# Performance work log

Measured on AMD Instinct MI355X. Metric: run time of the kernel, lower is better.

The kernel has to match this reference:

```python
import jax, jax.numpy as jnp
import numpy as np

K = 20          # neighbors
EPS = 1e-5      # BatchNorm eps (eval mode, running_mean=0, running_var=1)
SLOPE = 0.01    # LeakyReLU default negative_slope


def lrelu(v):
    return jnp.where(v >= 0, v, SLOPE * v)


def bn4d(y, g, b):  # y: (B, C, N, k) or (B, C, N)
    shape = (1, g.shape[0]) + (1,) * (y.ndim - 2)
    return y * (g / jnp.sqrt(1.0 + EPS)).reshape(shape) + b.reshape(shape)


def knn_idx(x, k):  # x: (B, C, N) -> (B, N, k) indices of k nearest points
    xx = jnp.sum(x * x, axis=1)                      # (B, N)
    inner = jnp.einsum('bcn,bcm->bnm', x, x)         # (B, N, N)
    dist = 2.0 * inner - xx[:, :, None] - xx[:, None, :]  # = -||xi-xj||^2
    _, idx = jax.lax.top_k(dist, k)
    return idx


def graph_feature(x, k):  # x: (B, C, N) -> (B, 2C, N, k)
    idx = knn_idx(x, k)                              # (B, N, k)
    xt = jnp.transpose(x, (0, 2, 1))                 # (B, N, C)
    nbr = jax.vmap(lambda p, i: p[i])(xt, idx)       # (B, N, k, C) gather
    ctr = xt[:, :, None, :]                          # (B, N, 1, C)
    feat = jnp.concatenate([nbr - ctr, jnp.broadcast_to(ctr, nbr.shape)], axis=-1)
    return jnp.transpose(feat, (0, 3, 1, 2))         # (B, 2C, N, k)


def edge_conv(x, w, g, b, bias=None):  # 1x1 conv + BN(eval) + LeakyReLU + max over k
    f = graph_feature(x, K)                          # (B, 2C, N, k)
    y = jnp.einsum('oc,bcnk->bonk', w, f)
    if bias is not None:
        y = y + bias.reshape(1, -1, 1, 1)
    return jnp.max(lrelu(bn4d(y, g, b)), axis=-1)    # (B, O, N)


def setup_inputs() -> dict:
    key = jax.random.key(0)
    ks = jax.random.split(key, 24)
    W = lambda k_, o, c: jax.random.normal(k_, (o, c), jnp.float32) / np.sqrt(c)
    g = lambda k_, c: 1.0 + 0.1 * jax.random.normal(k_, (c,), jnp.float32)
    bt = lambda k_, c: 0.1 * jax.random.normal(k_, (c,), jnp.float32)
    return {
        'x': jax.random.normal(ks[0], (8, 1024, 3), jnp.float32),
        'conv1_w': W(ks[1], 64, 6), 'conv1_b': bt(ks[2], 64),
        'bn1_g': g(ks[3], 64), 'bn1_b': bt(ks[4], 64),
        'conv2_w': W(ks[5], 64, 128), 'bn2_g': g(ks[6], 64), 'bn2_b': bt(ks[7], 64),
        'conv3_w': W(ks[8], 128, 128), 'bn3_g': g(ks[9], 128), 'bn3_b': bt(ks[10], 128),
        'conv4_w': W(ks[11], 256, 256), 'bn4_g': g(ks[12], 256), 'bn4_b': bt(ks[13], 256),
        'conv5_w': W(ks[14], 1024, 512),
        'lin1_w': W(ks[15], 512, 1024), 'bn6_g': g(ks[16], 512), 'bn6_b': bt(ks[17], 512),
        'lin2_w': W(ks[18], 256, 512), 'lin2_b': bt(ks[19], 256),
        'bn7_g': g(ks[20], 256), 'bn7_b': bt(ks[21], 256),
        'lin3_w': W(ks[22], 40, 256), 'lin3_b': bt(ks[23], 40),
    }


def reference(x, conv1_w, conv1_b, bn1_g, bn1_b, conv2_w, bn2_g, bn2_b,
              conv3_w, bn3_g, bn3_b, conv4_w, bn4_g, bn4_b, conv5_w,
              lin1_w, bn6_g, bn6_b, lin2_w, lin2_b, bn7_g, bn7_b, lin3_w, lin3_b):
    p = jnp.transpose(x, (0, 2, 1))                  # (B, 3, N)
    x1 = edge_conv(p, conv1_w, bn1_g, bn1_b, bias=conv1_b)   # (B, 64, N)
    x2 = edge_conv(x1, conv2_w, bn2_g, bn2_b)                # (B, 64, N)
    x3 = edge_conv(x2, conv3_w, bn3_g, bn3_b)                # (B, 128, N)
    x4 = edge_conv(x3, conv4_w, bn4_g, bn4_b)                # (B, 256, N)
    xc = jnp.concatenate([x1, x2, x3, x4], axis=1)           # (B, 512, N)
    e = jnp.einsum('oc,bcn->bon', conv5_w, xc)               # (B, 1024, N); bn5 unused in original forward
    gpool = jnp.max(e, axis=-1)                              # (B, 1024) adaptive_max_pool1d(1)
    y = gpool @ lin1_w.T
    y = lrelu(y * (bn6_g / jnp.sqrt(1.0 + EPS)) + bn6_b)     # dropout = identity (eval)
    y = y @ lin2_w.T + lin2_b
    y = lrelu(y * (bn7_g / jnp.sqrt(1.0 + EPS)) + bn7_b)
    return y @ lin3_w.T + lin3_b                             # (B, num_classes)
```

## Files before the change

kernel.cpp:

```cpp
#include <hip/hip_runtime.h>
#include <cmath>
#include <cstdint>
#include <cstddef>

#define NB 8
#define NPTS 1024
#define BN (NB*NPTS)
#define KNN 20
#define XC_C 512
#define BN_SC 0.99999500003749973f

static __device__ __forceinline__ float lrelu(float z) { return z >= 0.f ? z : 0.01f * z; }

template<int CTRL>
static __device__ __forceinline__ void dpp_max2(unsigned& loA, unsigned& hiA,
                                                unsigned& loB, unsigned& hiB) {
    unsigned tlA = (unsigned)__builtin_amdgcn_update_dpp(0, (int)loA, CTRL, 0xF, 0xF, false);
    unsigned thA = (unsigned)__builtin_amdgcn_update_dpp(0, (int)hiA, CTRL, 0xF, 0xF, false);
    unsigned tlB = (unsigned)__builtin_amdgcn_update_dpp(0, (int)loB, CTRL, 0xF, 0xF, false);
    unsigned thB = (unsigned)__builtin_amdgcn_update_dpp(0, (int)hiB, CTRL, 0xF, 0xF, false);
    unsigned long long a = ((unsigned long long)hiA << 32) | loA;
    unsigned long long b = ((unsigned long long)thA << 32) | tlA;
    if (b > a) { loA = tlA; hiA = thA; }
    unsigned long long c = ((unsigned long long)hiB << 32) | loB;
    unsigned long long d = ((unsigned long long)thB << 32) | tlB;
    if (d > c) { loB = tlB; hiB = thB; }
}

static __device__ __forceinline__ void wave_max_u64_x2(unsigned long long vA, unsigned long long vB,
                                                       unsigned long long& winA, unsigned long long& winB) {
    unsigned loA = (unsigned)vA, hiA = (unsigned)(vA >> 32);
    unsigned loB = (unsigned)vB, hiB = (unsigned)(vB >> 32);
    dpp_max2<0x121>(loA, hiA, loB, hiB);
    dpp_max2<0x122>(loA, hiA, loB, hiB);
    dpp_max2<0x124>(loA, hiA, loB, hiB);
    dpp_max2<0x128>(loA, hiA, loB, hiB);
    dpp_max2<0x142>(loA, hiA, loB, hiB);
    dpp_max2<0x143>(loA, hiA, loB, hiB);
    unsigned wloA = (unsigned)__builtin_amdgcn_readlane((int)loA, 63);
    unsigned whiA = (unsigned)__builtin_amdgcn_readlane((int)hiA, 63);
    unsigned wloB = (unsigned)__builtin_amdgcn_readlane((int)loB, 63);
    unsigned whiB = (unsigned)__builtin_amdgcn_readlane((int)hiB, 63);
    winA = ((unsigned long long)whiA << 32) | wloA;
    winB = ((unsigned long long)whiB << 32) | wloB;
}

static __device__ __forceinline__ unsigned long long shflx64(unsigned long long v, int m) {
    int lo = __shfl_xor((int)(unsigned)v, m);
    int hi = __shfl_xor((int)(unsigned)(v >> 32), m);
    return ((unsigned long long)(unsigned)hi << 32) | (unsigned)lo;
}

static __device__ __forceinline__ unsigned long long rdlane64(unsigned long long v, int l) {
    unsigned lo = (unsigned)__builtin_amdgcn_readlane((int)(unsigned)v, l);
    unsigned hi = (unsigned)__builtin_amdgcn_readlane((int)(unsigned)(v >> 32), l);
    return ((unsigned long long)hi << 32) | lo;
}

static __device__ __forceinline__ void bitonic64_desc_x2(unsigned long long& vA,
                                                         unsigned long long& vB, int lane) {
#pragma unroll
    for (int k = 2; k <= 64; k <<= 1) {
#pragma unroll
        for (int j = k >> 1; j > 0; j >>= 1) {
            unsigned long long pA = shflx64(vA, j);
            unsigned long long pB = shflx64(vB, j);
            bool takeMax = (((lane & k) == 0) == ((lane & j) == 0));
            vA = ((pA > vA) == takeMax) ? pA : vA;
            vB = ((pB > vB) == takeMax) ? pB : vB;
        }
    }
}

static __device__ __forceinline__ void select_pair(const float4* accA, const float4* accB,
                                                   const float4* nm4, int lane,
                                                   unsigned long long (*cw)[64],
                                                   int rA, int rB, int* __restrict__ idx) {
    unsigned long long keyA[16], keyB[16];
#pragma unroll
    for (int j = 0; j < 4; j++) {
        float4 nm = nm4[lane + 64*j];
#pragma unroll
        for (int q = 0; q < 4; q++) {
            int m = 4*(lane + 64*j) + q;
            float fA = 2.f * (&accA[j].x)[q] - (&nm.x)[q];
            unsigned uA = __float_as_uint(fA);
            unsigned sA_ = (unsigned)((int)uA >> 31);
            uA ^= (sA_ | 0x80000000u);
            keyA[4*j+q] = ((unsigned long long)uA << 32) | (unsigned)(1023 - m);
            float fB = 2.f * (&accB[j].x)[q] - (&nm.x)[q];
            unsigned uB = __float_as_uint(fB);
            unsigned sB_ = (unsigned)((int)uB >> 31);
            uB ^= (sB_ | 0x80000000u);
            keyB[4*j+q] = ((unsigned long long)uB << 32) | (unsigned)(1023 - m);
        }
    }

    unsigned long long hA = keyA[0], hB = keyB[0];
#pragma unroll
    for (int i = 1; i < 16; i++) {
        hA = keyA[i] > hA ? keyA[i] : hA;
        hB = keyB[i] > hB ? keyB[i] : hB;
    }

    unsigned long long shA = hA, shB = hB;
    bitonic64_desc_x2(shA, shB, lane);
    unsigned long long LA = rdlane64(shA, KNN - 1);
    unsigned long long LB = rdlane64(shB, KNN - 1);

    int cA = 0, cB = 0;
#pragma unroll
    for (int i = 0; i < 16; i++) {
        cA += (keyA[i] >= LA) ? 1 : 0;
        cB += (keyB[i] >= LB) ? 1 : 0;
    }
    int sA = cA, sB = cB;
#pragma unroll
    for (int off = 1; off < 64; off <<= 1) {
        int tA = __shfl_up(sA, off);
        int tB = __shfl_up(sB, off);
        if (lane >= off) { sA += tA; sB += tB; }
    }
    int totA = __builtin_amdgcn_readlane(sA, 63);
    int totB = __builtin_amdgcn_readlane(sB, 63);
    int pA = sA - cA, pB = sB - cB;

    if (totA <= 64 && totB <= 64) {
        int wa = pA, wb = pB;
#pragma unroll
        for (int i = 0; i < 16; i++) {
            if (keyA[i] >= LA) cw[0][wa++] = keyA[i];
            if (keyB[i] >= LB) cw[1][wb++] = keyB[i];
        }
        asm volatile("s_waitcnt lgkmcnt(0)" ::: "memory");
        unsigned long long vA = 0ull, vB = 0ull;
        if (lane < totA) vA = cw[0][lane];
        if (lane < totB) vB = cw[1][lane];
        bitonic64_desc_x2(vA, vB, lane);
        if (lane < KNN) {
            idx[rA * KNN + lane] = 1023 - (int)(unsigned)vA;
            idx[rB * KNN + lane] = 1023 - (int)(unsigned)vB;
        }
    } else {
#pragma unroll
        for (int ksz = 2; ksz <= 16; ksz <<= 1) {
#pragma unroll
            for (int jst = ksz >> 1; jst > 0; jst >>= 1) {
#pragma unroll
                for (int i = 0; i < 16; i++) {
                    int l = i ^ jst;
                    if (l > i) {
                        bool dsc = (i & ksz) == 0;
                        unsigned long long a = keyA[i], bbv = keyA[l];
                        bool swA = dsc ? (a < bbv) : (a > bbv);
                        if (swA) { keyA[i] = bbv; keyA[l] = a; }
                        unsigned long long c = keyB[i], d = keyB[l];
                        bool swB = dsc ? (c < d) : (c > d);
                        if (swB) { keyB[i] = d; keyB[l] = c; }
                    }
                }
            }
        }
        int mineA = 0, mineB = 0;
        for (int kk = 0; kk < KNN; kk++) {
            unsigned long long winA, winB;
            wave_max_u64_x2(keyA[0], keyB[0], winA, winB);
            if (lane == kk) {
                mineA = 1023 - (int)(unsigned)winA;
                mineB = 1023 - (int)(unsigned)winB;
            }
            bool popA = (keyA[0] == winA);
            bool popB = (keyB[0] == winB);
#pragma unroll
            for (int t = 0; t < 15; t++) {
                keyA[t] = popA ? keyA[t+1] : keyA[t];
                keyB[t] = popB ? keyB[t+1] : keyB[t];
            }
            keyA[15] = popA ? 0ull : keyA[15];
            keyB[15] = popB ? 0ull : keyB[15];
        }
        if (lane < KNN) {
            idx[rA * KNN + lane] = mineA;
            idx[rB * KNN + lane] = mineB;
        }
    }
}

static __device__ __forceinline__ unsigned short f2bf(float f) {
    unsigned u = __float_as_uint(f);
    unsigned r = u + 0x7fffu + ((u >> 16) & 1u);
    return (unsigned short)(r >> 16);
}
static __device__ __forceinline__ float bf2f(unsigned short h) {
    return __uint_as_float(((unsigned)h) << 16);
}

typedef __attribute__((ext_vector_type(8))) short short8;
typedef __attribute__((ext_vector_type(4))) float floatx4;

__global__ void prep_k(const float* __restrict__ x, float* __restrict__ ft, float* __restrict__ nrm) {
    int i = blockIdx.x * 256 + threadIdx.x;
    if (i >= BN) return;
    int b = i >> 10, n = i & 1023;
    float a = x[3*i], c = x[3*i+1], d = x[3*i+2];
    float* fb = ft + (size_t)b * 3 * NPTS;
    fb[n] = a; fb[NPTS + n] = c; fb[2*NPTS + n] = d;
    nrm[i] = a*a + c*c + d*d;
}

template<int C, int R>
__global__ __launch_bounds__(256, 2) void knn_k(const float* __restrict__ ft,
                                                const float* __restrict__ frow, int frs,
                                                const float* __restrict__ nrm,
                                                int* __restrict__ idx) {
    __shared__ unsigned long long cand[4][2][64];
    __shared__ float sbuf[((C & 3) == 0) ? 2 * 4 * NPTS : 1];
    int tid = threadIdx.x;
    int w = tid >> 6;
    int lane = tid & 63;
    int b    = blockIdx.x & 7;
    int slot = blockIdx.x >> 3;
    int r0 = b * NPTS + slot * (4*R) + R * w;
    const float* ftb = ft + (size_t)b * C * NPTS;

    float4 acc[R][4];
#pragma unroll
    for (int rr = 0; rr < R; rr++)
#pragma unroll
        for (int j = 0; j < 4; j++) acc[rr][j] = make_float4(0.f,0.f,0.f,0.f);

    if constexpr ((C & 3) == 0) {
        constexpr int NC = C / 4;
        const float4* cr0 = (const float4*)(frow + (size_t)r0 * frs);
        int frs4 = frs >> 2;
        const float4* src4 = (const float4*)ftb;
        float* sbase = &sbuf[0];
        float4 pf[4];
#pragma unroll
        for (int i = 0; i < 4; i++) pf[i] = src4[i*256 + tid];
        {
            float4* sw = (float4*)sbase;
#pragma unroll
            for (int i = 0; i < 4; i++) sw[i*256 + tid] = pf[i];
        }
        __syncthreads();
        for (int c4 = 0; c4 < NC; c4++) {
            int cur = c4 & 1;
            if (c4 + 1 < NC) {
#pragma unroll
                for (int i = 0; i < 4; i++) pf[i] = src4[(size_t)(4*(c4+1)+i)*256 + tid];
            }
            float4 ct[R];
#pragma unroll
            for (int rr = 0; rr < R; rr++) ct[rr] = cr0[c4 + rr*frs4];
            const float4* sc = (const float4*)(sbase + cur * 4 * NPTS);
#pragma unroll
            for (int cc = 0; cc < 4; cc++) {
                const float4* rm = sc + cc*256;
#pragma unroll
                for (int j = 0; j < 4; j++) {
                    float4 v = rm[lane + 64*j];
#pragma unroll
                    for (int rr = 0; rr < R; rr++) {
                        float cs = (&ct[rr].x)[cc];
                        acc[rr][j].x = fmaf(cs, v.x, acc[rr][j].x);
                        acc[rr][j].y = fmaf(cs, v.y, acc[rr][j].y);
                        acc[rr][j].z = fmaf(cs, v.z, acc[rr][j].z);
                        acc[rr][j].w = fmaf(cs, v.w, acc[rr][j].w);
                    }
                }
            }
            if (c4 + 1 < NC) {
                float4* sw = (float4*)(sbase + (cur ^ 1) * 4 * NPTS);
#pragma unroll
                for (int i = 0; i < 4; i++) sw[i*256 + tid] = pf[i];
                __syncthreads();
            }
        }
    } else {
        for (int c = 0; c < C; c++) {
            float ct[R];
#pragma unroll
            for (int rr = 0; rr < R; rr++) ct[rr] = frow[(size_t)(r0+rr) * frs + c];
            const float4* rm = (const float4*)(ftb + (size_t)c * NPTS);
#pragma unroll
            for (int j = 0; j < 4; j++) {
                float4 v = rm[lane + 64*j];
#pragma unroll
                for (int rr = 0; rr < R; rr++) {
                    float cs = ct[rr];
                    acc[rr][j].x = fmaf(cs, v.x, acc[rr][j].x);
                    acc[rr][j].y = fmaf(cs, v.y, acc[rr][j].y);
                    acc[rr][j].z = fmaf(cs, v.z, acc[rr][j].z);
                    acc[rr][j].w = fmaf(cs, v.w, acc[rr][j].w);
                }
            }
        }
    }

    const float4* nm4 = (const float4*)(nrm + b * NPTS);
#pragma unroll
    for (int p = 0; p < R/2; p++)
        select_pair(acc[2*p], acc[2*p+1], nm4, lane, cand[w], r0 + 2*p, r0 + 2*p + 1, idx);
}

template<int C, int O, bool HASB, int RPB>
__global__ void hc_k(const float* __restrict__ F, int FS,
                     const float* __restrict__ w, const float* __restrict__ bias,
                     float* __restrict__ Ht, float* __restrict__ Ct) {
    int r0 = blockIdx.x * RPB;
    int o = threadIdx.x;
    const float* wr = w + (size_t)o * (2*C);
    float h[RPB], a2[RPB];
#pragma unroll
    for (int nn = 0; nn < RPB; nn++) { h[nn] = 0.f; a2[nn] = 0.f; }
    if constexpr ((C & 3) == 0) {
        const float4* w1 = (const float4*)wr;
        const float4* w2 = (const float4*)(wr + C);
#pragma unroll 4
        for (int c4 = 0; c4 < C/4; c4++) {
            float4 wa = w1[c4], wb = w2[c4];
#pragma unroll
            for (int nn = 0; nn < RPB; nn++) {
                float4 f = *(const float4*)(F + (size_t)(r0+nn)*FS + 4*c4);
                h[nn]  = fmaf(wa.x,f.x, fmaf(wa.y,f.y, fmaf(wa.z,f.z, fmaf(wa.w,f.w, h[nn]))));
                a2[nn] = fmaf(wb.x,f.x, fmaf(wb.y,f.y, fmaf(wb.z,f.z, fmaf(wb.w,f.w, a2[nn]))));
            }
        }
    } else {
        for (int c = 0; c < C; c++) {
            float wa = wr[c], wb = wr[C+c];
#pragma unroll
            for (int nn = 0; nn < RPB; nn++) {
                float f = F[(size_t)(r0+nn)*FS + c];
                h[nn]  = fmaf(wa, f, h[nn]);
                a2[nn] = fmaf(wb, f, a2[nn]);
            }
        }
    }
    float bs = 0.f;
    if constexpr (HASB) bs = bias[o];
#pragma unroll
    for (int nn = 0; nn < RPB; nn++) {
        size_t ro = (size_t)(r0+nn)*O + o;
        Ht[ro] = h[nn];
        Ct[ro] = a2[nn] - h[nn] + bs;
    }
}

template<int O, bool WFT>
__global__ void gmax_k(const float* __restrict__ Ht, const float* __restrict__ Ct,
                       const int* __restrict__ idx,
                       const float* __restrict__ g, const float* __restrict__ bb,
                       float* __restrict__ xcs, float* __restrict__ ft, float* __restrict__ nrm) {
    int b = blockIdx.x & 7;
    int n = blockIdx.x >> 3;
    int r = b * NPTS + n;
    int o = threadIdx.x;
    const int* id = idx + r * KNN;
    float vmax = -INFINITY, vmin = INFINITY;
    const float* hb = Ht + (size_t)b * NPTS * O + o;
#pragma unroll 4
    for (int k = 0; k < KNN; k++) {
        int m = id[k];
        float v = hb[(size_t)m * O];
        vmax = fmaxf(vmax, v); vmin = fminf(vmin, v);
    }
    float ct = Ct[(size_t)r * O + o];
    float s = g[o] * BN_SC;
    float pre = (s >= 0.f ? vmax : vmin) + ct;
    float out = lrelu(fmaf(s, pre, bb[o]));
    xcs[(size_t)r * XC_C + o] = out;
    if constexpr (WFT) {
        ft[((size_t)b * O + o) * NPTS + n] = out;
        float sq = out * out;
#pragma unroll
        for (int off = 32; off > 0; off >>= 1) sq += __shfl_xor(sq, off);
        __shared__ float red[O/64 > 0 ? O/64 : 1];
        if ((o & 63) == 0) red[o >> 6] = sq;
        __syncthreads();
        if (o == 0) {
            float t = 0.f;
#pragma unroll
            for (int i = 0; i < O/64; i++) t += red[i];
            nrm[r] = t;
        }
    }
}

__global__ void xcvt_k(const float* __restrict__ xc,
                       unsigned short* __restrict__ xh, unsigned short* __restrict__ xl) {
    int i = blockIdx.x * 256 + threadIdx.x;
    float v = xc[i];
    unsigned short h = f2bf(v);
    xh[i] = h;
    xl[i] = f2bf(v - bf2f(h));
}

__global__ void wcvt_k(const float* __restrict__ w5,
                       unsigned short* __restrict__ wh, unsigned short* __restrict__ wl) {
    int i = blockIdx.x * 256 + threadIdx.x;
    float v = w5[i];
    unsigned short h = f2bf(v);
    wh[i] = h;
    wl[i] = f2bf(v - bf2f(h));
}

__global__ __launch_bounds__(256) void conv5mfma_k(const unsigned short* __restrict__ xh,
                                                   const unsigned short* __restrict__ xl,
                                                   const unsigned short* __restrict__ wh,
                                                   const unsigned short* __restrict__ wl,
                                                   float* __restrict__ part) {
    __shared__ short ah_s[32*72];
    __shared__ short al_s[32*72];
    __shared__ short bh_s[128*72];
    __shared__ short bl_s[128*72];
    int b = blockIdx.z, og = blockIdx.y, nt = blockIdx.x;
    int tid = threadIdx.x;
    int w = tid >> 6, lane = tid & 63;
    int m = lane & 15, quad = lane >> 4;
    int h = w >> 1, q = w & 1;
    size_t nbase = (size_t)b * NPTS + nt * 32;
    int obase = og * 128;
    int srow = tid >> 3;
    int scol = (tid & 7) * 8;

    floatx4 acc[4];
#pragma unroll
    for (int t = 0; t < 4; t++) acc[t] = (floatx4){0.f, 0.f, 0.f, 0.f};

    for (int kc = 0; kc < 512; kc += 64) {
        short8 pa[2], pb[8];
        pa[0] = *(const short8*)(xh + (nbase + srow)*512 + kc + scol);
        pa[1] = *(const short8*)(xl + (nbase + srow)*512 + kc + scol);
#pragma unroll
        for (int i = 0; i < 4; i++) {
            int r = srow + i*32;
            pb[2*i]   = *(const short8*)(wh + (size_t)(obase + r)*512 + kc + scol);
            pb[2*i+1] = *(const short8*)(wl + (size_t)(obase + r)*512 + kc + scol);
        }
        __syncthreads();
        *(short8*)(ah_s + srow*72 + scol) = pa[0];
        *(short8*)(al_s + srow*72 + scol) = pa[1];
#pragma unroll
        for (int i = 0; i < 4; i++) {
            int r = srow + i*32;
            *(short8*)(bh_s + r*72 + scol) = pb[2*i];
            *(short8*)(bl_s + r*72 + scol) = pb[2*i+1];
        }
        __syncthreads();
#pragma unroll
        for (int kk = 0; kk < 2; kk++) {
            short8 ah8 = *(const short8*)(ah_s + (h*16 + m)*72 + kk*32 + quad*8);
            short8 al8 = *(const short8*)(al_s + (h*16 + m)*72 + kk*32 + quad*8);
#pragma unroll
            for (int t = 0; t < 4; t++) {
                short8 bh8 = *(const short8*)(bh_s + (q*64 + t*16 + m)*72 + kk*32 + quad*8);
                short8 bl8 = *(const short8*)(bl_s + (q*64 + t*16 + m)*72 + kk*32 + quad*8);
                acc[t] = __builtin_amdgcn_mfma_f32_16x16x32_bf16(ah8, bh8, acc[t], 0, 0, 0);
                acc[t] = __builtin_amdgcn_mfma_f32_16x16x32_bf16(ah8, bl8, acc[t], 0, 0, 0);
                acc[t] = __builtin_amdgcn_mfma_f32_16x16x32_bf16(al8, bh8, acc[t], 0, 0, 0);
            }
        }
    }
#pragma unroll
    for (int t = 0; t < 4; t++) {
        float v = fmaxf(fmaxf(acc[t][0], acc[t][1]), fmaxf(acc[t][2], acc[t][3]));
        v = fmaxf(v, __shfl_xor(v, 16));
        v = fmaxf(v, __shfl_xor(v, 32));
        if (quad == 0)
            part[((size_t)b * 64 + nt*2 + h) * 1024 + obase + q*64 + t*16 + m] = v;
    }
}

__global__ void gpool_k(const float* __restrict__ part, float* __restrict__ gp) {
    int i = blockIdx.x * 256 + threadIdx.x;
    int b = i >> 10, o = i & 1023;
    const float* pb = part + (size_t)b * 64 * 1024 + o;
    float m = pb[0];
#pragma unroll 4
    for (int j = 1; j < 64; j++) m = fmaxf(m, pb[(size_t)j * 1024]);
    gp[i] = m;
}

template<int C, bool HASBIAS, bool ACT>
__global__ __launch_bounds__(256) void lin_k(const float* __restrict__ X, int xs,
                                             const float* __restrict__ W,
                                             const float* __restrict__ bias,
                                             const float* __restrict__ g, const float* __restrict__ bb,
                                             float* __restrict__ Y, int ys) {
    int wid = (blockIdx.x * 256 + threadIdx.x) >> 6;
    int lane = threadIdx.x & 63;
    int o = wid >> 3;
    int b = wid & 7;
    const float4* wr = (const float4*)(W + (size_t)o * C);
    const float4* xr = (const float4*)(X + (size_t)b * xs);
    float acc = 0.f;
#pragma unroll
    for (int i = 0; i < C/256; i++) {
        float4 w = wr[lane + 64*i];
        float4 xv = xr[lane + 64*i];
        acc = fmaf(w.x,xv.x, fmaf(w.y,xv.y, fmaf(w.z,xv.z, fmaf(w.w,xv.w, acc))));
    }
#pragma unroll
    for (int off = 32; off > 0; off >>= 1) acc += __shfl_xor(acc, off);
    if (lane == 0) {
        if constexpr (HASBIAS) acc += bias[o];
        if constexpr (ACT) acc = lrelu(fmaf(acc, g[o] * BN_SC, bb[o]));
        Y[(size_t)b * ys + o] = acc;
    }
}

extern "C" void kernel_launch(void* const* d_in, const int* in_sizes, int n_in,
                              void* d_out, int out_size, void* d_ws, size_t ws_size,
                              hipStream_t stream) {
    const float* x       = (const float*)d_in[0];
    const float* conv1_w = (const float*)d_in[1];
    const float* conv1_b = (const float*)d_in[2];
    const float* bn1_g   = (const float*)d_in[3];
    const float* bn1_b   = (const float*)d_in[4];
    const float* conv2_w = (const float*)d_in[5];
    const float* bn2_g   = (const float*)d_in[6];
    const float* bn2_b   = (const float*)d_in[7];
    const float* conv3_w = (const float*)d_in[8];
    const float* bn3_g   = (const float*)d_in[9];
    const float* bn3_b   = (const float*)d_in[10];
    const float* conv4_w = (const float*)d_in[11];
    const float* bn4_g   = (const float*)d_in[12];
    const float* bn4_b   = (const float*)d_in[13];
    const float* conv5_w = (const float*)d_in[14];
    const float* lin1_w  = (const float*)d_in[15];
    const float* bn6_g   = (const float*)d_in[16];
    const float* bn6_b   = (const float*)d_in[17];
    const float* lin2_w  = (const float*)d_in[18];
    const float* lin2_b  = (const float*)d_in[19];
    const float* bn7_g   = (const float*)d_in[20];
    const float* bn7_b   = (const float*)d_in[21];
    const float* lin3_w  = (const float*)d_in[22];
    const float* lin3_b  = (const float*)d_in[23];
    float* outp = (float*)d_out;

    float* ws   = (float*)d_ws;
    float* xc   = ws;
    int*   idxb = (int*)(ws + 4194304);
    float* nrm  = ws + 4194304 + 163840;
    float* ft   = nrm + 8192;
    float* part = ft + 1048576;
    float* w5t  = part + 524288;
    float* Ht   = w5t + 524288;
    float* Ct   = Ht + 2097152;
    float* gp   = ft;
    float* y1   = ft + 8192;
    float* y2   = ft + 8192 + 4096;
    unsigned short* xhp = (unsigned short*)Ht;
    unsigned short* xlp = (unsigned short*)Ct;
    unsigned short* whp = (unsigned short*)w5t;
    unsigned short* wlp = whp + 1024*512;

    prep_k<<<BN/256, 256, 0, stream>>>(x, ft, nrm);

    knn_k<3, 2><<<BN/8, 256, 0, stream>>>(ft, x, 3, nrm, idxb);
    hc_k<3, 64, true, 4><<<BN/4, 64, 0, stream>>>(x, 3, conv1_w, conv1_b, Ht, Ct);
    gmax_k<64, true><<<BN, 64, 0, stream>>>(Ht, Ct, idxb, bn1_g, bn1_b, xc + 0, ft, nrm);

    knn_k<64, 2><<<BN/8, 256, 0, stream>>>(ft, xc + 0, XC_C, nrm, idxb);
    hc_k<64, 64, false, 4><<<BN/4, 64, 0, stream>>>(xc + 0, XC_C, conv2_w, nullptr, Ht, Ct);
    gmax_k<64, true><<<BN, 64, 0, stream>>>(Ht, Ct, idxb, bn2_g, bn2_b, xc + 64, ft, nrm);

    knn_k<64, 2><<<BN/8, 256, 0, stream>>>(ft, xc + 64, XC_C, nrm, idxb);
    hc_k<64, 128, false, 4><<<BN/4, 128, 0, stream>>>(xc + 64, XC_C, conv3_w, nullptr, Ht, Ct);
    gmax_k<128, true><<<BN, 128, 0, stream>>>(Ht, Ct, idxb, bn3_g, bn3_b, xc + 128, ft, nrm);

    knn_k<128, 2><<<BN/8, 256, 0, stream>>>(ft, xc + 128, XC_C, nrm, idxb);
    hc_k<128, 256, false, 8><<<BN/8, 256, 0, stream>>>(xc + 128, XC_C, conv4_w, nullptr, Ht, Ct);
    gmax_k<256, false><<<BN, 256, 0, stream>>>(Ht, Ct, idxb, bn4_g, bn4_b, xc + 256, nullptr, nullptr);

    xcvt_k<<<BN*512/256, 256, 0, stream>>>(xc, xhp, xlp);
    wcvt_k<<<1024*512/256, 256, 0, stream>>>(conv5_w, whp, wlp);
    conv5mfma_k<<<dim3(32, 8, NB), 256, 0, stream>>>(xhp, xlp, whp, wlp, part);
    gpool_k<<<NB*1024/256, 256, 0, stream>>>(part, gp);
    lin_k<1024, false, true><<<NB*512/4, 256, 0, stream>>>(gp, 1024, lin1_w, nullptr, bn6_g, bn6_b, y1, 512);
    lin_k<512,  true,  true><<<NB*256/4, 256, 0, stream>>>(y1, 512, lin2_w, lin2_b, bn7_g, bn7_b, y2, 256);
    lin_k<256,  true, false><<<NB*40/4,  256, 0, stream>>>(y2, 256, lin3_w, lin3_b, nullptr, nullptr, outp, 40);
}
```

Baseline: 427.5 us.

## Raise kNN rows per wave and co-launch last kNN with conv4 projection

Each kNN wave now handles four query rows instead of two, halving the grid and reusing each loaded shared-memory tile across more rows. The layer-4 kNN and the conv4 per-point projection, which are independent, are merged into one launch whose blocks branch on block index. This removes one launch and lets the two workloads overlap on the GPU. In exchange, doubling the per-thread accumulators raises register pressure under the 2-blocks launch bound, and the hc blocks in the merged kernel reserve the full kNN shared-memory buffer, which can lower occupancy.

```diff
diff --git a/kernel.cpp b/kernel.cpp
--- a/kernel.cpp
+++ b/kernel.cpp
@@ -186,6 +186,181 @@
     }
 }
 
+template<int C, int R>
+static __device__ __forceinline__ void knn_body(int blk,
+                                                const float* __restrict__ ft,
+                                                const float* __restrict__ frow, int frs,
+                                                const float* __restrict__ nrm,
+                                                int* __restrict__ idx,
+                                                unsigned long long (*cand)[2][64],
+                                                float* sbuf) {
+    int tid = threadIdx.x;
+    int w = tid >> 6;
+    int lane = tid & 63;
+    int b    = blk & 7;
+    int slot = blk >> 3;
+    int r0 = b * NPTS + slot * (4*R) + R * w;
+    const float* ftb = ft + (size_t)b * C * NPTS;
+
+    float4 acc[R][4];
+#pragma unroll
+    for (int rr = 0; rr < R; rr++)
+#pragma unroll
+        for (int j = 0; j < 4; j++) acc[rr][j] = make_float4(0.f,0.f,0.f,0.f);
+
+    if constexpr ((C & 3) == 0) {
+        constexpr int NC = C / 4;
+        const float4* cr0 = (const float4*)(frow + (size_t)r0 * frs);
+        int frs4 = frs >> 2;
+        const float4* src4 = (const float4*)ftb;
+        float4 pf[4];
+#pragma unroll
+        for (int i = 0; i < 4; i++) pf[i] = src4[i*256 + tid];
+        {
+            float4* sw = (float4*)sbuf;
+#pragma unroll
+            for (int i = 0; i < 4; i++) sw[i*256 + tid] = pf[i];
+        }
+        __syncthreads();
+        for (int c4 = 0; c4 < NC; c4++) {
+            int cur = c4 & 1;
+            if (c4 + 1 < NC) {
+#pragma unroll
+                for (int i = 0; i < 4; i++) pf[i] = src4[(size_t)(4*(c4+1)+i)*256 + tid];
+            }
+            float4 ct[R];
+#pragma unroll
+            for (int rr = 0; rr < R; rr++) ct[rr] = cr0[c4 + rr*frs4];
+            const float4* sc = (const float4*)(sbuf + cur * 4 * NPTS);
+#pragma unroll
+            for (int cc = 0; cc < 4; cc++) {
+                const float4* rm = sc + cc*256;
+#pragma unroll
+                for (int j = 0; j < 4; j++) {
+                    float4 v = rm[lane + 64*j];
+#pragma unroll
+                    for (int rr = 0; rr < R; rr++) {
+                        float cs = (&ct[rr].x)[cc];
+                        acc[rr][j].x = fmaf(cs, v.x, acc[rr][j].x);
+                        acc[rr][j].y = fmaf(cs, v.y, acc[rr][j].y);
+                        acc[rr][j].z = fmaf(cs, v.z, acc[rr][j].z);
+                        acc[rr][j].w = fmaf(cs, v.w, acc[rr][j].w);
+                    }
+                }
+            }
+            if (c4 + 1 < NC) {
+                float4* sw = (float4*)(sbuf + (cur ^ 1) * 4 * NPTS);
+#pragma unroll
+                for (int i = 0; i < 4; i++) sw[i*256 + tid] = pf[i];
+                __syncthreads();
+            }
+        }
+    } else {
+        for (int c = 0; c < C; c++) {
+            float ct[R];
+#pragma unroll
+            for (int rr = 0; rr < R; rr++) ct[rr] = frow[(size_t)(r0+rr) * frs + c];
+            const float4* rm = (const float4*)(ftb + (size_t)c * NPTS);
+#pragma unroll
+            for (int j = 0; j < 4; j++) {
+                float4 v = rm[lane + 64*j];
+#pragma unroll
+                for (int rr = 0; rr < R; rr++) {
+                    float cs = ct[rr];
+                    acc[rr][j].x = fmaf(cs, v.x, acc[rr][j].x);
+                    acc[rr][j].y = fmaf(cs, v.y, acc[rr][j].y);
+                    acc[rr][j].z = fmaf(cs, v.z, acc[rr][j].z);
+                    acc[rr][j].w = fmaf(cs, v.w, acc[rr][j].w);
+                }
+            }
+        }
+    }
+
+    const float4* nm4 = (const float4*)(nrm + b * NPTS);
+#pragma unroll
+    for (int p = 0; p < R/2; p++)
+        select_pair(acc[2*p], acc[2*p+1], nm4, lane, cand[w], r0 + 2*p, r0 + 2*p + 1, idx);
+}
+
+template<int C, int R>
+__global__ __launch_bounds__(256, 2) void knn_k(const float* __restrict__ ft,
+                                                const float* __restrict__ frow, int frs,
+                                                const float* __restrict__ nrm,
+                                                int* __restrict__ idx) {
+    __shared__ unsigned long long cand[4][2][64];
+    __shared__ float sbuf[((C & 3) == 0) ? 2 * 4 * NPTS : 1];
+    knn_body<C, R>(blockIdx.x, ft, frow, frs, nrm, idx, cand, &sbuf[0]);
+}
+
+template<int C, int O, bool HASB, int RPB>
+static __device__ __forceinline__ void hc_body(int blk,
+                                               const float* __restrict__ F, int FS,
+                                               const float* __restrict__ w, const float* __restrict__ bias,
+                                               float* __restrict__ Ht, float* __restrict__ Ct) {
+    int r0 = blk * RPB;
+    int o = threadIdx.x;
+    const float* wr = w + (size_t)o * (2*C);
+    float h[RPB], a2[RPB];
+#pragma unroll
+    for (int nn = 0; nn < RPB; nn++) { h[nn] = 0.f; a2[nn] = 0.f; }
+    if constexpr ((C & 3) == 0) {
+        const float4* w1 = (const float4*)wr;
+        const float4* w2 = (const float4*)(wr + C);
+#pragma unroll 4
+        for (int c4 = 0; c4 < C/4; c4++) {
+            float4 wa = w1[c4], wb = w2[c4];
+#pragma unroll
+            for (int nn = 0; nn < RPB; nn++) {
+                float4 f = *(const float4*)(F + (size_t)(r0+nn)*FS + 4*c4);
+                h[nn]  = fmaf(wa.x,f.x, fmaf(wa.y,f.y, fmaf(wa.z,f.z, fmaf(wa.w,f.w, h[nn]))));
+                a2[nn] = fmaf(wb.x,f.x, fmaf(wb.y,f.y, fmaf(wb.z,f.z, fmaf(wb.w,f.w, a2[nn]))));
+            }
+        }
+    } else {
+        for (int c = 0; c < C; c++) {
+            float wa = wr[c], wb = wr[C+c];
+#pragma unroll
+            for (int nn = 0; nn < RPB; nn++) {
+                float f = F[(size_t)(r0+nn)*FS + c];
+                h[nn]  = fmaf(wa, f, h[nn]);
+                a2[nn] = fmaf(wb, f, a2[nn]);
+            }
+        }
+    }
+    float bs = 0.f;
+    if constexpr (HASB) bs = bias[o];
+#pragma unroll
+    for (int nn = 0; nn < RPB; nn++) {
+        size_t ro = (size_t)(r0+nn)*O + o;
+        Ht[ro] = h[nn];
+        Ct[ro] = a2[nn] - h[nn] + bs;
+    }
+}
+
+template<int C, int O, bool HASB, int RPB>
+__global__ void hc_k(const float* __restrict__ F, int FS,
+                     const float* __restrict__ w, const float* __restrict__ bias,
+                     float* __restrict__ Ht, float* __restrict__ Ct) {
+    hc_body<C, O, HASB, RPB>(blockIdx.x, F, FS, w, bias, Ht, Ct);
+}
+
+template<int C, int R, int O, int RPB>
+__global__ __launch_bounds__(256, 2) void knnhc_k(const float* __restrict__ ft,
+                                                  const float* __restrict__ frow, int frs,
+                                                  const float* __restrict__ nrm,
+                                                  int* __restrict__ idx,
+                                                  const float* __restrict__ w4,
+                                                  float* __restrict__ Ht, float* __restrict__ Ct,
+                                                  int knnBlocks) {
+    __shared__ unsigned long long cand[4][2][64];
+    __shared__ float sbuf[2 * 4 * NPTS];
+    if ((int)blockIdx.x < knnBlocks) {
+        knn_body<C, R>(blockIdx.x, ft, frow, frs, nrm, idx, cand, &sbuf[0]);
+    } else {
+        hc_body<C, O, false, RPB>(blockIdx.x - knnBlocks, frow, frs, w4, nullptr, Ht, Ct);
+    }
+}
+
 static __device__ __forceinline__ unsigned short f2bf(float f) {
     unsigned u = __float_as_uint(f);
     unsigned r = u + 0x7fffu + ((u >> 16) & 1u);
@@ -206,146 +381,6 @@
     float* fb = ft + (size_t)b * 3 * NPTS;
     fb[n] = a; fb[NPTS + n] = c; fb[2*NPTS + n] = d;
     nrm[i] = a*a + c*c + d*d;
-}
-
-template<int C, int R>
-__global__ __launch_bounds__(256, 2) void knn_k(const float* __restrict__ ft,
-                                                const float* __restrict__ frow, int frs,
-                                                const float* __restrict__ nrm,
-                                                int* __restrict__ idx) {
-    __shared__ unsigned long long cand[4][2][64];
-    __shared__ float sbuf[((C & 3) == 0) ? 2 * 4 * NPTS : 1];
-    int tid = threadIdx.x;
-    int w = tid >> 6;
-    int lane = tid & 63;
-    int b    = blockIdx.x & 7;
-    int slot = blockIdx.x >> 3;
-    int r0 = b * NPTS + slot * (4*R) + R * w;
-    const float* ftb = ft + (size_t)b * C * NPTS;
-
-    float4 acc[R][4];
-#pragma unroll
-    for (int rr = 0; rr < R; rr++)
-#pragma unroll
-        for (int j = 0; j < 4; j++) acc[rr][j] = make_float4(0.f,0.f,0.f,0.f);
-
-    if constexpr ((C & 3) == 0) {
-        constexpr int NC = C / 4;
-        const float4* cr0 = (const float4*)(frow + (size_t)r0 * frs);
-        int frs4 = frs >> 2;
-        const float4* src4 = (const float4*)ftb;
-        float* sbase = &sbuf[0];
-        float4 pf[4];
-#pragma unroll
-        for (int i = 0; i < 4; i++) pf[i] = src4[i*256 + tid];
-        {
-            float4* sw = (float4*)sbase;
-#pragma unroll
-            for (int i = 0; i < 4; i++) sw[i*256 + tid] = pf[i];
-        }
-        __syncthreads();
-        for (int c4 = 0; c4 < NC; c4++) {
-            int cur = c4 & 1;
-            if (c4 + 1 < NC) {
-#pragma unroll
-                for (int i = 0; i < 4; i++) pf[i] = src4[(size_t)(4*(c4+1)+i)*256 + tid];
-            }
-            float4 ct[R];
-#pragma unroll
-            for (int rr = 0; rr < R; rr++) ct[rr] = cr0[c4 + rr*frs4];
-            const float4* sc = (const float4*)(sbase + cur * 4 * NPTS);
-#pragma unroll
-            for (int cc = 0; cc < 4; cc++) {
-                const float4* rm = sc + cc*256;
-#pragma unroll
-                for (int j = 0; j < 4; j++) {
-                    float4 v = rm[lane + 64*j];
-#pragma unroll
-                    for (int rr = 0; rr < R; rr++) {
-                        float cs = (&ct[rr].x)[cc];
-                        acc[rr][j].x = fmaf(cs, v.x, acc[rr][j].x);
-                        acc[rr][j].y = fmaf(cs, v.y, acc[rr][j].y);
-                        acc[rr][j].z = fmaf(cs, v.z, acc[rr][j].z);
-                        acc[rr][j].w = fmaf(cs, v.w, acc[rr][j].w);
-                    }
-                }
-            }
-            if (c4 + 1 < NC) {
-                float4* sw = (float4*)(sbase + (cur ^ 1) * 4 * NPTS);
-#pragma unroll
-                for (int i = 0; i < 4; i++) sw[i*256 + tid] = pf[i];
-                __syncthreads();
-            }
-        }
-    } else {
-        for (int c = 0; c < C; c++) {
-            float ct[R];
-#pragma unroll
-            for (int rr = 0; rr < R; rr++) ct[rr] = frow[(size_t)(r0+rr) * frs + c];
-            const float4* rm = (const float4*)(ftb + (size_t)c * NPTS);
-#pragma unroll
-            for (int j = 0; j < 4; j++) {
-                float4 v = rm[lane + 64*j];
-#pragma unroll
-                for (int rr = 0; rr < R; rr++) {
-                    float cs = ct[rr];
-                    acc[rr][j].x = fmaf(cs, v.x, acc[rr][j].x);
-                    acc[rr][j].y = fmaf(cs, v.y, acc[rr][j].y);
-                    acc[rr][j].z = fmaf(cs, v.z, acc[rr][j].z);
-                    acc[rr][j].w = fmaf(cs, v.w, acc[rr][j].w);
-                }
-            }
-        }
-    }
-
-    const float4* nm4 = (const float4*)(nrm + b * NPTS);
-#pragma unroll
-    for (int p = 0; p < R/2; p++)
-        select_pair(acc[2*p], acc[2*p+1], nm4, lane, cand[w], r0 + 2*p, r0 + 2*p + 1, idx);
-}
-
-template<int C, int O, bool HASB, int RPB>
-__global__ void hc_k(const float* __restrict__ F, int FS,
-                     const float* __restrict__ w, const float* __restrict__ bias,
-                     float* __restrict__ Ht, float* __restrict__ Ct) {
-    int r0 = blockIdx.x * RPB;
-    int o = threadIdx.x;
-    const float* wr = w + (size_t)o * (2*C);
-    float h[RPB], a2[RPB];
-#pragma unroll
-    for (int nn = 0; nn < RPB; nn++) { h[nn] = 0.f; a2[nn] = 0.f; }
-    if constexpr ((C & 3) == 0) {
-        const float4* w1 = (const float4*)wr;
-        const float4* w2 = (const float4*)(wr + C);
-#pragma unroll 4
-        for (int c4 = 0; c4 < C/4; c4++) {
-            float4 wa = w1[c4], wb = w2[c4];
-#pragma unroll
-            for (int nn = 0; nn < RPB; nn++) {
-                float4 f = *(const float4*)(F + (size_t)(r0+nn)*FS + 4*c4);
-                h[nn]  = fmaf(wa.x,f.x, fmaf(wa.y,f.y, fmaf(wa.z,f.z, fmaf(wa.w,f.w, h[nn]))));
-                a2[nn] = fmaf(wb.x,f.x, fmaf(wb.y,f.y, fmaf(wb.z,f.z, fmaf(wb.w,f.w, a2[nn]))));
-            }
-        }
-    } else {
-        for (int c = 0; c < C; c++) {
-            float wa = wr[c], wb = wr[C+c];
-#pragma unroll
-            for (int nn = 0; nn < RPB; nn++) {
-                float f = F[(size_t)(r0+nn)*FS + c];
-                h[nn]  = fmaf(wa, f, h[nn]);
-                a2[nn] = fmaf(wb, f, a2[nn]);
-            }
-        }
-    }
-    float bs = 0.f;
-    if constexpr (HASB) bs = bias[o];
-#pragma unroll
-    for (int nn = 0; nn < RPB; nn++) {
-        size_t ro = (size_t)(r0+nn)*O + o;
-        Ht[ro] = h[nn];
-        Ct[ro] = a2[nn] - h[nn] + bs;
-    }
 }
 
 template<int O, bool WFT>
@@ -559,20 +594,20 @@
 
     prep_k<<<BN/256, 256, 0, stream>>>(x, ft, nrm);
 
-    knn_k<3, 2><<<BN/8, 256, 0, stream>>>(ft, x, 3, nrm, idxb);
+    knn_k<3, 4><<<BN/16, 256, 0, stream>>>(ft, x, 3, nrm, idxb);
     hc_k<3, 64, true, 4><<<BN/4, 64, 0, stream>>>(x, 3, conv1_w, conv1_b, Ht, Ct);
     gmax_k<64, true><<<BN, 64, 0, stream>>>(Ht, Ct, idxb, bn1_g, bn1_b, xc + 0, ft, nrm);
 
-    knn_k<64, 2><<<BN/8, 256, 0, stream>>>(ft, xc + 0, XC_C, nrm, idxb);
+    knn_k<64, 4><<<BN/16, 256, 0, stream>>>(ft, xc + 0, XC_C, nrm, idxb);
     hc_k<64, 64, false, 4><<<BN/4, 64, 0, stream>>>(xc + 0, XC_C, conv2_w, nullptr, Ht, Ct);
     gmax_k<64, true><<<BN, 64, 0, stream>>>(Ht, Ct, idxb, bn2_g, bn2_b, xc + 64, ft, nrm);
 
-    knn_k<64, 2><<<BN/8, 256, 0, stream>>>(ft, xc + 64, XC_C, nrm, idxb);
+    knn_k<64, 4><<<BN/16, 256, 0, stream>>>(ft, xc + 64, XC_C, nrm, idxb);
     hc_k<64, 128, false, 4><<<BN/4, 128, 0, stream>>>(xc + 64, XC_C, conv3_w, nullptr, Ht, Ct);
     gmax_k<128, true><<<BN, 128, 0, stream>>>(Ht, Ct, idxb, bn3_g, bn3_b, xc + 128, ft, nrm);
 
-    knn_k<128, 2><<<BN/8, 256, 0, stream>>>(ft, xc + 128, XC_C, nrm, idxb);
-    hc_k<128, 256, false, 8><<<BN/8, 256, 0, stream>>>(xc + 128, XC_C, conv4_w, nullptr, Ht, Ct);
+    knnhc_k<128, 4, 256, 8><<<BN/16 + BN/8, 256, 0, stream>>>(ft, xc + 128, XC_C, nrm, idxb,
+                                                              conv4_w, Ht, Ct, BN/16);
     gmax_k<256, false><<<BN, 256, 0, stream>>>(Ht, Ct, idxb, bn4_g, bn4_b, xc + 256, nullptr, nullptr);
 
     xcvt_k<<<BN*512/256, 256, 0, stream>>>(xc, xhp, xlp);
```

Result: faster. 392.2 us, median of 3 (-8.3%).
